# Performance work log

Hardware: AMD Instinct MI355X
Metric: run time of the kernel (lower is better)

## Reference

```python
import jax, jax.numpy as jnp
from jax import lax
import numpy as np

B, CIN, HC, K, REC = 64, 64, 64, 3, 5
MG = 240 // REC  # 48
EPS = 1e-8


def conv2d(x, w, b, pad):
    y = lax.conv_general_dilated(x, w, (1, 1), [(pad, pad), (pad, pad)],
                                 dimension_numbers=('NCHW', 'OIHW', 'NCHW'))
    return y + b[None, :, None, None]


def conv_transpose2d(x, w, b, stride, pad):
    # PyTorch ConvTranspose2d: w is (Cin, Cout, kH, kW)
    k = w.shape[2]
    w_t = jnp.transpose(w[:, :, ::-1, ::-1], (1, 0, 2, 3))  # -> OIHW, flipped
    y = lax.conv_general_dilated(x, w_t, (1, 1),
                                 [(k - 1 - pad, k - 1 - pad)] * 2,
                                 lhs_dilation=(stride, stride),
                                 dimension_numbers=('NCHW', 'OIHW', 'NCHW'))
    return y + b[None, :, None, None]


def leaky(x):
    return jnp.where(x >= 0, x, 0.2 * x)


def setup_inputs() -> dict:
    key = jax.random.key(0)
    ks = jax.random.split(key, 12)
    s = 0.05
    return {
        'x': jax.random.normal(ks[0], (B, CIN, 64, 64), jnp.float32),
        'h': jax.random.normal(ks[1], (B, HC, 64, 64), jnp.float32),
        'c': jax.random.normal(ks[2], (B, HC, 64, 64), jnp.float32),
        'recalled_memory_feature': jax.random.normal(ks[3], (B, REC, MG, 32, 32), jnp.float32),
        'conv_w': jax.random.normal(ks[4], (5 * HC, CIN + HC, K, K), jnp.float32) * s,
        'conv_b': jax.random.normal(ks[5], (5 * HC,), jnp.float32) * s,
        'convc_w': jax.random.normal(ks[6], (MG, HC, 1, 1), jnp.float32) * s,
        'convc_b': jax.random.normal(ks[7], (MG,), jnp.float32) * s,
        'convssm_w': jax.random.normal(ks[8], (MG, MG, 4, 4), jnp.float32) * s,
        'convssm_b': jax.random.normal(ks[9], (MG,), jnp.float32) * s,
        'convfuse_w': jax.random.normal(ks[10], (HC, MG + HC, 1, 1), jnp.float32) * s,
        'convfuse_b': jax.random.normal(ks[11], (HC,), jnp.float32) * s,
    }


def reference(x, h, c, recalled_memory_feature, conv_w, conv_b, convc_w, convc_b,
              convssm_w, convssm_b, convfuse_w, convfuse_b):
    rm = recalled_memory_feature.reshape(B, REC, MG, 32, 32)
    rm_avg = rm.mean(axis=(3, 4))                      # (B, REC, MG)
    q = leaky(conv2d(c, convc_w, convc_b, 0))          # (B, MG, 64, 64)
    q_avg = q.mean(axis=(2, 3))                        # (B, MG)
    # cosine similarity along channel dim, vectorized over (B, REC)
    qn = jnp.maximum(jnp.linalg.norm(q_avg, axis=1, keepdims=True), EPS)   # (B,1)
    mn = jnp.maximum(jnp.linalg.norm(rm_avg, axis=2), EPS)                  # (B,REC)
    cos = jnp.einsum('bm,brm->br', q_avg, rm_avg) / (qn * mn)               # (B,REC)
    attn = jax.nn.softmax(cos, axis=1)                                      # (B,REC)
    mt = jnp.einsum('br,brmhw->bmhw', attn, rm)        # (B, MG, 32, 32)
    mt = leaky(conv_transpose2d(mt, convssm_w, convssm_b, 2, 1))  # (B, MG, 64, 64)

    gates = conv2d(jnp.concatenate((x, h), axis=1), conv_w, conv_b, K // 2)
    i, f, g, o, lam = jnp.split(gates, 5, axis=1)
    i = jax.nn.sigmoid(i)
    f = jax.nn.sigmoid(f)
    o = jax.nn.sigmoid(o)
    g = jnp.tanh(g)
    lam = jax.nn.sigmoid(lam)
    c_new = f * c + i * g
    h_new = o * jnp.tanh(conv2d(jnp.concatenate((c_new, mt), axis=1), convfuse_w, convfuse_b, 0))
    h_out = lam * h_new + (1.0 - lam) * h
    return (h_out, c_new)
```

## Files before the change

### kernel.cpp

```cpp
#include <hip/hip_runtime.h>
#include <hip/hip_bf16.h>
#include <cstdint>

#define HW 4096
#define MGc 48
#define RECc 5

typedef __attribute__((ext_vector_type(8))) short bf16x8;
typedef __attribute__((ext_vector_type(4))) float f32x4;

__device__ __forceinline__ float sigf(float x) { return 1.f / (1.f + expf(-x)); }
__device__ __forceinline__ float leakyf(float x) { return x >= 0.f ? x : 0.2f * x; }
__device__ __forceinline__ unsigned short f2bfu(float f) {
  __hip_bfloat16 b = __float2bfloat16(f);
  return *reinterpret_cast<unsigned short*>(&b);
}
__device__ __forceinline__ float bfu2f(unsigned short u) {
  unsigned v = ((unsigned)u) << 16;
  return __uint_as_float(v);
}
__device__ __forceinline__ void gload_lds16(const void* g, void* l) {
  __builtin_amdgcn_global_load_lds(
      (const __attribute__((address_space(1))) unsigned int*)g,
      (__attribute__((address_space(3))) unsigned int*)l, 16, 0, 0);
}

__global__ __launch_bounds__(256) void k_rm_sum(const float* __restrict__ rm,
                                                float* __restrict__ rm_sum) {
  int row = blockIdx.x;
  const float4* p = reinterpret_cast<const float4*>(rm + (size_t)row * 1024);
  float4 v = p[threadIdx.x];
  float s = v.x + v.y + v.z + v.w;
  #pragma unroll
  for (int off = 32; off; off >>= 1) s += __shfl_down(s, off);
  __shared__ float sred[4];
  if ((threadIdx.x & 63) == 0) sred[threadIdx.x >> 6] = s;
  __syncthreads();
  if (threadIdx.x == 0) rm_sum[row] = sred[0] + sred[1] + sred[2] + sred[3];
}

__global__ __launch_bounds__(256) void k_q_part(const float* __restrict__ c,
    const float* __restrict__ ccw, const float* __restrict__ ccb,
    float* __restrict__ q_part) {
  __shared__ float wl[MGc * 64];
  __shared__ float bl[MGc];
  __shared__ float red[4][MGc];
  int b = blockIdx.y, seg = blockIdx.x;
  for (int i = threadIdx.x; i < MGc * 64; i += 256) wl[i] = ccw[i];
  if (threadIdx.x < MGc) bl[threadIdx.x] = ccb[threadIdx.x];
  __syncthreads();
  int px = seg * 256 + threadIdx.x;
  float acc[MGc];
  #pragma unroll
  for (int m = 0; m < MGc; m++) acc[m] = 0.f;
  const float* cp = c + (size_t)b * 64 * HW + px;
  for (int ci = 0; ci < 64; ci++) {
    float v = cp[(size_t)ci * HW];
    #pragma unroll
    for (int m = 0; m < MGc; m++) acc[m] += wl[m * 64 + ci] * v;
  }
  int lane = threadIdx.x & 63, wv = threadIdx.x >> 6;
  #pragma unroll
  for (int m = 0; m < MGc; m++) {
    float t = leakyf(acc[m] + bl[m]);
    #pragma unroll
    for (int off = 32; off; off >>= 1) t += __shfl_down(t, off);
    if (lane == 0) red[wv][m] = t;
  }
  __syncthreads();
  if (threadIdx.x < MGc) {
    float t = red[0][threadIdx.x] + red[1][threadIdx.x] + red[2][threadIdx.x] + red[3][threadIdx.x];
    q_part[((size_t)b * 16 + seg) * MGc + threadIdx.x] = t;
  }
}

__global__ __launch_bounds__(256) void k_mt_pre(const float* __restrict__ rm,
    const float* __restrict__ rm_sum, const float* __restrict__ q_part,
    float* __restrict__ mt_pre) {
  __shared__ float sat[RECc];
  int idx = blockIdx.x * 256 + threadIdx.x;
  int b = idx / (MGc * 1024);
  if (threadIdx.x < 64) {
    int lane = threadIdx.x;
    float q = 0.f;
    if (lane < MGc) {
      float s = 0.f;
      for (int sg = 0; sg < 16; sg++) s += q_part[((size_t)b * 16 + sg) * MGc + lane];
      q = s * (1.f / 4096.f);
    }
    float qs = q * q;
    #pragma unroll
    for (int off = 32; off; off >>= 1) qs += __shfl_xor(qs, off);
    float qn = fmaxf(sqrtf(qs), 1e-8f);
    float cosv[RECc];
    #pragma unroll
    for (int r = 0; r < RECc; r++) {
      float m = 0.f;
      if (lane < MGc) m = rm_sum[((size_t)b * RECc + r) * MGc + lane] * (1.f / 1024.f);
      float d = q * m, ms = m * m;
      #pragma unroll
      for (int off = 32; off; off >>= 1) { d += __shfl_xor(d, off); ms += __shfl_xor(ms, off); }
      float mn = fmaxf(sqrtf(ms), 1e-8f);
      cosv[r] = d / (qn * mn);
    }
    float mx = cosv[0];
    #pragma unroll
    for (int r = 1; r < RECc; r++) mx = fmaxf(mx, cosv[r]);
    float ssum = 0.f;
    #pragma unroll
    for (int r = 0; r < RECc; r++) { cosv[r] = expf(cosv[r] - mx); ssum += cosv[r]; }
    float inv = 1.f / ssum;
    #pragma unroll
    for (int r = 0; r < RECc; r++)
      if (lane == r) sat[r] = cosv[r] * inv;
  }
  __syncthreads();
  int rem = idx - b * (MGc * 1024);
  const float* base = rm + (size_t)b * RECc * MGc * 1024 + rem;
  float v = sat[0] * base[0] + sat[1] * base[MGc * 1024] + sat[2] * base[2 * MGc * 1024]
          + sat[3] * base[3 * MGc * 1024] + sat[4] * base[4 * MGc * 1024];
  mt_pre[idx] = v;
}

__global__ __launch_bounds__(512) void k_ssm(const float* __restrict__ mt_pre,
    const float* __restrict__ w, const float* __restrict__ bias,
    __hip_bfloat16* __restrict__ mt) {
  __shared__ float in_t[12][10][20];
  __shared__ float w_t[12][48][16];
  int b = blockIdx.y;
  int tile = blockIdx.x;
  int y0 = (tile >> 1) * 16, x0 = (tile & 1) * 32;
  int wv = threadIdx.x >> 6, lane = threadIdx.x & 63;
  int co0 = wv * 6;
  int oyl = lane >> 2, xseg = lane & 3;
  int oy = y0 + oyl;
  int iy0 = (y0 >> 1) - 1, ix0 = (x0 >> 1) - 1;
  int kyA = (oy + 1) & 1;
  int iyA = (oy + 1 - kyA) >> 1;
  int rA = iyA - iy0, rB = rA - 1;
  float acc[6][8] = {};
  for (int ch = 0; ch < 4; ch++) {
    int ci0 = ch * 12;
    __syncthreads();
    for (int i = threadIdx.x; i < 12 * 10 * 18; i += 512) {
      int ci = i / 180, rr = (i % 180) / 18, cc2 = i % 18;
      int giy = iy0 + rr, gix = ix0 + cc2;
      float v = 0.f;
      if ((unsigned)giy < 32u && (unsigned)gix < 32u)
        v = mt_pre[(((size_t)b * MGc + ci0 + ci) * 32 + giy) * 32 + gix];
      in_t[ci][rr][cc2] = v;
    }
    for (int i = threadIdx.x; i < 12 * 48 * 16; i += 512)
      (&w_t[0][0][0])[i] = w[ci0 * 768 + i];
    __syncthreads();
    #pragma unroll 1
    for (int ci = 0; ci < 12; ci++) {
      float4 a0 = *reinterpret_cast<const float4*>(&in_t[ci][rA][xseg * 4]);
      float4 a1 = *reinterpret_cast<const float4*>(&in_t[ci][rA][xseg * 4 + 4]);
      float4 b0 = *reinterpret_cast<const float4*>(&in_t[ci][rB][xseg * 4]);
      float4 b1 = *reinterpret_cast<const float4*>(&in_t[ci][rB][xseg * 4 + 4]);
      float vA[6] = {a0.x, a0.y, a0.z, a0.w, a1.x, a1.y};
      float vB[6] = {b0.x, b0.y, b0.z, b0.w, b1.x, b1.y};
      #pragma unroll
      for (int co = 0; co < 6; co++) {
        const float* wp = &w_t[ci][co0 + co][0];
        float4 wA = *reinterpret_cast<const float4*>(wp + kyA * 4);
        float4 wB = *reinterpret_cast<const float4*>(wp + (kyA + 2) * 4);
        #pragma unroll
        for (int j = 0; j < 8; j++) {
          if ((j & 1) == 0) {
            int hi = (j >> 1) + 1, lo = j >> 1;
            acc[co][j] += vA[hi] * wA.y + vA[lo] * wA.w + vB[hi] * wB.y + vB[lo] * wB.w;
          } else {
            int hi = ((j + 1) >> 1) + 1, lo = (j + 1) >> 1;
            acc[co][j] += vA[hi] * wA.x + vA[lo] * wA.z + vB[hi] * wB.x + vB[lo] * wB.z;
          }
        }
      }
    }
  }
  int oxb = x0 + xseg * 8;
  #pragma unroll
  for (int co = 0; co < 6; co++) {
    float bb = bias[co0 + co];
    size_t obase = (((size_t)b * MGc + co0 + co) * 64 + oy) * 64 + oxb;
    #pragma unroll
    for (int j = 0; j < 8; j++)
      mt[obase + j] = __float2bfloat16(leakyf(acc[co][j] + bb));
  }
}

__global__ __launch_bounds__(256) void k_ppack(const float* __restrict__ xin,
    const float* __restrict__ hin, __hip_bfloat16* __restrict__ P) {
  __shared__ float t[64][65];
  int b = blockIdx.z, y = blockIdx.y, half = blockIdx.x;
  const float* src = (half ? hin : xin) + (size_t)b * 64 * HW + y * 64;
  #pragma unroll
  for (int it = 0; it < 4; it++) {
    int li = it * 256 + threadIdx.x;
    int ci = li >> 4, x4 = (li & 15) * 4;
    float4 v = *reinterpret_cast<const float4*>(src + (size_t)ci * HW + x4);
    t[x4][ci] = v.x; t[x4 + 1][ci] = v.y; t[x4 + 2][ci] = v.z; t[x4 + 3][ci] = v.w;
  }
  __syncthreads();
  int x = threadIdx.x >> 2, c16 = (threadIdx.x & 3) * 16;
  unsigned short* dst = reinterpret_cast<unsigned short*>(P) +
      (((size_t)b * 4096 + (size_t)y * 64 + x) * 128 + half * 64 + c16);
  bf16x8 o0, o1;
  #pragma unroll
  for (int j = 0; j < 8; j++) {
    o0[j] = (short)f2bfu(t[x][c16 + j]);
    o1[j] = (short)f2bfu(t[x][c16 + 8 + j]);
  }
  *reinterpret_cast<bf16x8*>(dst) = o0;
  *reinterpret_cast<bf16x8*>(dst + 8) = o1;
}

__global__ __launch_bounds__(256) void k_wpack(const float* __restrict__ cw,
                                               __hip_bfloat16* __restrict__ Wp) {
  int idx = blockIdx.x * 256 + threadIdx.x;
  if (idx >= 9 * 320 * 128) return;
  int t = idx / (320 * 128);
  int rem = idx % (320 * 128);
  int ocp = rem / 128, ci = rem % 128;
  int nt = ocp / 80, r2 = ocp % 80, gate = r2 / 16, ml = r2 % 16;
  int oc = gate * 64 + nt * 16 + ml;
  float v = cw[((size_t)oc * 128 + ci) * 9 + t];
  Wp[idx] = __float2bfloat16(v);
}

__global__ __launch_bounds__(512) void k_gates_mfma(
    const __hip_bfloat16* __restrict__ P, const __hip_bfloat16* __restrict__ Wp,
    const float* __restrict__ c, const float* __restrict__ cb,
    float* __restrict__ c_new, __hip_bfloat16* __restrict__ o_g,
    __hip_bfloat16* __restrict__ lam_g) {
  __shared__ bf16x8 s_in[18 * 4 * 66];
  __shared__ bf16x8 s_w[9 * 4 * 80];
  int orig = blockIdx.y * gridDim.x + blockIdx.x;
  int t_id = (orig & 7) * 128 + (orig >> 3);
  int b = t_id >> 4;
  int ytile = (t_id >> 2) & 3, nt = t_id & 3;
  int y0 = ytile * 16;
  int tid = threadIdx.x;
  int wv = tid >> 6, lane = tid & 63;
  int wr = wv >> 2, xw = wv & 3;
  int lane15 = lane & 15, lq = lane >> 4;

  f32x4 acc[8][5];
  #pragma unroll
  for (int i = 0; i < 8; i++)
    #pragma unroll
    for (int j = 0; j < 5; j++) acc[i][j] = (f32x4)0.f;

  const char* Pb = (const char*)P;
  const char* Wb = (const char*)Wp;

  for (int cc = 0; cc < 4; cc++) {
    __syncthreads();
    #pragma unroll 1
    for (int u = wv; u < 72; u += 8) {
      int L = u >> 2, g = u & 3;
      int y = y0 - 1 + L;
      bf16x8* dst = &s_in[u * 66];
      if ((unsigned)y < 64u) {
        const char* gp = Pb + ((((size_t)b * 4096 + (size_t)y * 64 + lane) * 128) + cc * 32 + g * 8) * 2;
        gload_lds16(gp, (void*)(dst + 1));
        if (lane < 2) dst[lane * 65] = (bf16x8)0;
      } else {
        dst[lane] = (bf16x8)0;
        if (lane < 2) dst[64 + lane] = (bf16x8)0;
      }
    }
    #pragma unroll 1
    for (int u = wv; u < 45; u += 8) {
      int e = u * 64 + lane;
      int t = e / 320, rem = e % 320;
      int g = rem / 80, ol = rem % 80;
      const char* gp = Wb + (((size_t)t * 320 + nt * 80 + ol) * 128 + cc * 32 + g * 8) * 2;
      gload_lds16(gp, (void*)&s_w[e]);
    }
    __syncthreads();

    #pragma unroll
    for (int dx = 0; dx < 3; dx++) {
      bf16x8 af[10];
      #pragma unroll
      for (int ri = 0; ri < 10; ri++) {
        int L = wr * 8 + ri;
        af[ri] = s_in[(L * 4 + lq) * 66 + (xw * 16 + lane15 + dx)];
      }
      #pragma unroll
      for (int ky = 0; ky < 3; ky++) {
        int t = ky * 3 + dx;
        bf16x8 bw[5];
        #pragma unroll
        for (int gg = 0; gg < 5; gg++)
          bw[gg] = s_w[(t * 4 + lq) * 80 + gg * 16 + lane15];
        #pragma unroll
        for (int rr = 0; rr < 8; rr++) {
          #pragma unroll
          for (int gg = 0; gg < 5; gg++)
            acc[rr][gg] = __builtin_amdgcn_mfma_f32_16x16x32_bf16(
                af[rr + ky], bw[gg], acc[rr][gg], 0, 0, 0);
        }
      }
    }
  }

  int m_hid = nt * 16 + lane15;
  float bi = cb[m_hid], bff = cb[64 + m_hid], bgg = cb[128 + m_hid],
        bo = cb[192 + m_hid], bl = cb[256 + m_hid];
  int xb = xw * 16 + lq * 4;
  size_t chofs = ((size_t)b * 64 + m_hid) * HW;
  #pragma unroll
  for (int rr = 0; rr < 8; rr++) {
    int y = y0 + wr * 8 + rr;
    size_t pofs = chofs + (size_t)y * 64 + xb;
    f32x4 cold = *reinterpret_cast<const f32x4*>(c + pofs);
    f32x4 cn;
    unsigned short ov[4], lv[4];
    #pragma unroll
    for (int e = 0; e < 4; e++) {
      float i_ = sigf(acc[rr][0][e] + bi);
      float f_ = sigf(acc[rr][1][e] + bff);
      float g_ = tanhf(acc[rr][2][e] + bgg);
      float o_ = sigf(acc[rr][3][e] + bo);
      float l_ = sigf(acc[rr][4][e] + bl);
      cn[e] = f_ * cold[e] + i_ * g_;
      ov[e] = f2bfu(o_);
      lv[e] = f2bfu(l_);
    }
    *reinterpret_cast<f32x4*>(c_new + pofs) = cn;
    ushort4 ovv = {ov[0], ov[1], ov[2], ov[3]};
    ushort4 lvv = {lv[0], lv[1], lv[2], lv[3]};
    *reinterpret_cast<ushort4*>(reinterpret_cast<unsigned short*>(o_g) + pofs) = ovv;
    *reinterpret_cast<ushort4*>(reinterpret_cast<unsigned short*>(lam_g) + pofs) = lvv;
  }
}

__global__ __launch_bounds__(256) void k_fuse(const float* __restrict__ c_new,
    const __hip_bfloat16* __restrict__ mt, const __hip_bfloat16* __restrict__ o_g,
    const __hip_bfloat16* __restrict__ lam_g, const float* __restrict__ h,
    const float* __restrict__ fw, const float* __restrict__ fb,
    float* __restrict__ h_out) {
  __shared__ float wl[112][64];
  int b = blockIdx.y, seg = blockIdx.x;
  for (int i = threadIdx.x; i < 112 * 64; i += 256) {
    int ci = i >> 6, co = i & 63;
    wl[ci][co] = fw[co * 112 + ci];
  }
  __syncthreads();
  int px = seg * 512 + threadIdx.x * 2;
  size_t bofs = (size_t)b * 64 * HW;
  float2 acc[64];
  #pragma unroll
  for (int co = 0; co < 64; co++) { float bv = fb[co]; acc[co].x = bv; acc[co].y = bv; }
  #pragma unroll 1
  for (int ci = 0; ci < 64; ci++) {
    float2 v = *reinterpret_cast<const float2*>(c_new + bofs + (size_t)ci * HW + px);
    #pragma unroll
    for (int c4 = 0; c4 < 16; c4++) {
      float4 w = *reinterpret_cast<const float4*>(&wl[ci][c4 * 4]);
      acc[c4 * 4 + 0].x += w.x * v.x; acc[c4 * 4 + 0].y += w.x * v.y;
      acc[c4 * 4 + 1].x += w.y * v.x; acc[c4 * 4 + 1].y += w.y * v.y;
      acc[c4 * 4 + 2].x += w.z * v.x; acc[c4 * 4 + 2].y += w.z * v.y;
      acc[c4 * 4 + 3].x += w.w * v.x; acc[c4 * 4 + 3].y += w.w * v.y;
    }
  }
  const unsigned short* mtu = reinterpret_cast<const unsigned short*>(mt);
  size_t mtofs = (size_t)b * MGc * HW + px;
  #pragma unroll 1
  for (int ci = 0; ci < 48; ci++) {
    unsigned u = *reinterpret_cast<const unsigned*>(mtu + mtofs + (size_t)ci * HW);
    float vx = bfu2f((unsigned short)(u & 0xffff));
    float vy = bfu2f((unsigned short)(u >> 16));
    #pragma unroll
    for (int c4 = 0; c4 < 16; c4++) {
      float4 w = *reinterpret_cast<const float4*>(&wl[64 + ci][c4 * 4]);
      acc[c4 * 4 + 0].x += w.x * vx; acc[c4 * 4 + 0].y += w.x * vy;
      acc[c4 * 4 + 1].x += w.y * vx; acc[c4 * 4 + 1].y += w.y * vy;
      acc[c4 * 4 + 2].x += w.z * vx; acc[c4 * 4 + 2].y += w.z * vy;
      acc[c4 * 4 + 3].x += w.w * vx; acc[c4 * 4 + 3].y += w.w * vy;
    }
  }
  const unsigned short* ou = reinterpret_cast<const unsigned short*>(o_g);
  const unsigned short* lu = reinterpret_cast<const unsigned short*>(lam_g);
  #pragma unroll
  for (int co = 0; co < 64; co++) {
    size_t ofs = bofs + (size_t)co * HW + px;
    unsigned uo = *reinterpret_cast<const unsigned*>(ou + ofs);
    unsigned ul = *reinterpret_cast<const unsigned*>(lu + ofs);
    float2 hv = *reinterpret_cast<const float2*>(h + ofs);
    float hnx = tanhf(acc[co].x), hny = tanhf(acc[co].y);
    float ox = bfu2f((unsigned short)(uo & 0xffff)), oy = bfu2f((unsigned short)(uo >> 16));
    float lx = bfu2f((unsigned short)(ul & 0xffff)), ly = bfu2f((unsigned short)(ul >> 16));
    float2 r;
    r.x = lx * (ox * hnx) + (1.f - lx) * hv.x;
    r.y = ly * (oy * hny) + (1.f - ly) * hv.y;
    *reinterpret_cast<float2*>(h_out + ofs) = r;
  }
}

extern "C" void kernel_launch(void* const* d_in, const int* in_sizes, int n_in,
                              void* d_out, int out_size, void* d_ws, size_t ws_size,
                              hipStream_t stream) {
  const float* x   = (const float*)d_in[0];
  const float* h   = (const float*)d_in[1];
  const float* c   = (const float*)d_in[2];
  const float* rm  = (const float*)d_in[3];
  const float* cw  = (const float*)d_in[4];
  const float* cb  = (const float*)d_in[5];
  const float* ccw = (const float*)d_in[6];
  const float* ccb = (const float*)d_in[7];
  const float* sw  = (const float*)d_in[8];
  const float* sb  = (const float*)d_in[9];
  const float* fw  = (const float*)d_in[10];
  const float* fb  = (const float*)d_in[11];

  float* h_out = (float*)d_out;
  float* c_new = h_out + (size_t)16777216;

  char* ws = (char*)d_ws;
  float* rm_sum = (float*)(ws + 0);
  float* q_part = (float*)(ws + 65536);
  float* mt_pre = (float*)(ws + 327680);
  __hip_bfloat16* mt    = (__hip_bfloat16*)(ws + 12910592);
  __hip_bfloat16* o_g   = (__hip_bfloat16*)(ws + 38076416);
  __hip_bfloat16* lam_g = (__hip_bfloat16*)(ws + 71630848);
  __hip_bfloat16* P     = (__hip_bfloat16*)(ws + 105185280);
  __hip_bfloat16* Wp    = (__hip_bfloat16*)(ws + 172294144);

  k_wpack<<<1440, 256, 0, stream>>>(cw, Wp);
  k_ppack<<<dim3(2, 64, 64), 256, 0, stream>>>(x, h, P);
  k_rm_sum<<<15360, 256, 0, stream>>>(rm, rm_sum);
  k_q_part<<<dim3(16, 64), 256, 0, stream>>>(c, ccw, ccb, q_part);
  k_mt_pre<<<12288, 256, 0, stream>>>(rm, rm_sum, q_part, mt_pre);
  k_ssm<<<dim3(8, 64), 512, 0, stream>>>(mt_pre, sw, sb, mt);
  k_gates_mfma<<<dim3(16, 64), 512, 0, stream>>>(P, Wp, c, cb, c_new, o_g, lam_g);
  k_fuse<<<dim3(8, 64), 256, 0, stream>>>(c_new, mt, o_g, lam_g, h, fw, fb, h_out);
}
```

Baseline: 691.7 us.

## Double-buffer gates conv LDS staging with repacked tap-channel K dimension

Splits the channel reduction into eight 16-channel chunks staged into two LDS buffers, so the next chunk's global-to-LDS loads overlap MFMA compute on the current one. The K dimension of each MFMA is repacked to combine (tap, 8-channel group) pairs, with the final slot partially zeroed. MFMA bursts are wrapped in raised wave priority. This adds redundant zero MFMAs and more LDS fragment reads in exchange for hiding load latency.

```diff
diff --git a/kernel.cpp b/kernel.cpp
--- a/kernel.cpp
+++ b/kernel.cpp
@@ -234,8 +234,8 @@
     const float* __restrict__ c, const float* __restrict__ cb,
     float* __restrict__ c_new, __hip_bfloat16* __restrict__ o_g,
     __hip_bfloat16* __restrict__ lam_g) {
-  __shared__ bf16x8 s_in[18 * 4 * 66];
-  __shared__ bf16x8 s_w[9 * 4 * 80];
+  __shared__ bf16x8 s_in[2][36 * 66];
+  __shared__ bf16x8 s_w[2][18 * 80];
   int orig = blockIdx.y * gridDim.x + blockIdx.x;
   int t_id = (orig & 7) * 128 + (orig >> 3);
   int b = t_id >> 4;
@@ -245,6 +245,19 @@
   int wv = tid >> 6, lane = tid & 63;
   int wr = wv >> 2, xw = wv & 3;
   int lane15 = lane & 15, lq = lane >> 4;
+  int rowu = wr * 8;
+
+  int afq[5], bwq[5];
+  #pragma unroll
+  for (int q = 0; q < 5; q++) {
+    int j = q * 4 + lq;
+    int jj = (j < 18) ? j : (j - 2);
+    int t = jj >> 1, g = jj & 1;
+    int ky = t / 3, dx = t % 3;
+    afq[q] = ky * 132 + g * 66 + xw * 16 + lane15 + dx;
+    bwq[q] = (t * 2 + g) * 80 + lane15;
+  }
+  bool a4ok = (lq < 2);
 
   f32x4 acc[8][5];
   #pragma unroll
@@ -255,57 +268,72 @@
   const char* Pb = (const char*)P;
   const char* Wb = (const char*)Wp;
 
-  for (int cc = 0; cc < 4; cc++) {
+#define STAGE_K(BUF, CC) do {                                                         \
+    _Pragma("unroll 1")                                                               \
+    for (int u = wv; u < 36; u += 8) {                                                \
+      int L = u >> 1, g = u & 1;                                                      \
+      int y = y0 - 1 + L;                                                             \
+      bf16x8* dst = &s_in[BUF][u * 66];                                               \
+      if ((unsigned)y < 64u) {                                                        \
+        const char* gp = Pb + ((((size_t)b * 4096 + (size_t)y * 64 + lane) * 128)     \
+                               + (CC) * 16 + g * 8) * 2;                              \
+        gload_lds16(gp, (void*)(dst + 1));                                            \
+        if (lane < 2) dst[lane * 65] = (bf16x8)0;                                     \
+      } else {                                                                        \
+        dst[lane] = (bf16x8)0;                                                        \
+        if (lane < 2) dst[64 + lane] = (bf16x8)0;                                     \
+      }                                                                               \
+    }                                                                                 \
+    _Pragma("unroll 1")                                                               \
+    for (int u = wv; u < 23; u += 8) {                                                \
+      int e = u * 64 + lane;                                                          \
+      if (e < 1440) {                                                                 \
+        int unit = e / 80, ol = e % 80;                                               \
+        int t = unit >> 1, g = unit & 1;                                              \
+        const char* gp = Wb + (((size_t)t * 320 + nt * 80 + ol) * 128                 \
+                               + (CC) * 16 + g * 8) * 2;                              \
+        gload_lds16(gp, (void*)&s_w[BUF][e]);                                         \
+      }                                                                               \
+    }                                                                                 \
+  } while (0)
+
+#define COMPUTE_K(BUF) do {                                                           \
+    _Pragma("unroll")                                                                 \
+    for (int q = 0; q < 5; q++) {                                                     \
+      bf16x8 af[8];                                                                   \
+      _Pragma("unroll")                                                               \
+      for (int rr = 0; rr < 8; rr++) {                                                \
+        bf16x8 v = s_in[BUF][(rowu + rr) * 132 + afq[q]];                             \
+        af[rr] = (q < 4 || a4ok) ? v : (bf16x8)0;                                     \
+      }                                                                               \
+      bf16x8 bw[5];                                                                   \
+      _Pragma("unroll")                                                               \
+      for (int gg = 0; gg < 5; gg++) bw[gg] = s_w[BUF][bwq[q] + gg * 16];             \
+      __builtin_amdgcn_s_setprio(1);                                                  \
+      _Pragma("unroll")                                                               \
+      for (int rr = 0; rr < 8; rr++)                                                  \
+        _Pragma("unroll")                                                             \
+        for (int gg = 0; gg < 5; gg++)                                                \
+          acc[rr][gg] = __builtin_amdgcn_mfma_f32_16x16x32_bf16(                      \
+              af[rr], bw[gg], acc[rr][gg], 0, 0, 0);                                  \
+      __builtin_amdgcn_s_setprio(0);                                                  \
+    }                                                                                 \
+  } while (0)
+
+  STAGE_K(0, 0);
+  __syncthreads();
+  #pragma unroll 1
+  for (int cp = 0; cp < 4; cp++) {
+    int cc = cp * 2;
+    STAGE_K(1, cc + 1);
+    COMPUTE_K(0);
     __syncthreads();
-    #pragma unroll 1
-    for (int u = wv; u < 72; u += 8) {
-      int L = u >> 2, g = u & 3;
-      int y = y0 - 1 + L;
-      bf16x8* dst = &s_in[u * 66];
-      if ((unsigned)y < 64u) {
-        const char* gp = Pb + ((((size_t)b * 4096 + (size_t)y * 64 + lane) * 128) + cc * 32 + g * 8) * 2;
-        gload_lds16(gp, (void*)(dst + 1));
-        if (lane < 2) dst[lane * 65] = (bf16x8)0;
-      } else {
-        dst[lane] = (bf16x8)0;
-        if (lane < 2) dst[64 + lane] = (bf16x8)0;
-      }
-    }
-    #pragma unroll 1
-    for (int u = wv; u < 45; u += 8) {
-      int e = u * 64 + lane;
-      int t = e / 320, rem = e % 320;
-      int g = rem / 80, ol = rem % 80;
-      const char* gp = Wb + (((size_t)t * 320 + nt * 80 + ol) * 128 + cc * 32 + g * 8) * 2;
-      gload_lds16(gp, (void*)&s_w[e]);
-    }
+    if (cp < 3) STAGE_K(0, cc + 2);
+    COMPUTE_K(1);
     __syncthreads();
-
-    #pragma unroll
-    for (int dx = 0; dx < 3; dx++) {
-      bf16x8 af[10];
-      #pragma unroll
-      for (int ri = 0; ri < 10; ri++) {
-        int L = wr * 8 + ri;
-        af[ri] = s_in[(L * 4 + lq) * 66 + (xw * 16 + lane15 + dx)];
-      }
-      #pragma unroll
-      for (int ky = 0; ky < 3; ky++) {
-        int t = ky * 3 + dx;
-        bf16x8 bw[5];
-        #pragma unroll
-        for (int gg = 0; gg < 5; gg++)
-          bw[gg] = s_w[(t * 4 + lq) * 80 + gg * 16 + lane15];
-        #pragma unroll
-        for (int rr = 0; rr < 8; rr++) {
-          #pragma unroll
-          for (int gg = 0; gg < 5; gg++)
-            acc[rr][gg] = __builtin_amdgcn_mfma_f32_16x16x32_bf16(
-                af[rr + ky], bw[gg], acc[rr][gg], 0, 0, 0);
-        }
-      }
-    }
-  }
+  }
+#undef STAGE_K
+#undef COMPUTE_K
 
   int m_hid = nt * 16 + lane15;
   float bi = cb[m_hid], bff = cb[64 + m_hid], bgg = cb[128 + m_hid],
```

After: 785.9 us. +13.6%, slower.

## Load gate-conv input fragments directly from padded global layout, skip LDS staging

Applied to the files above, without the earlier changes.

The packed x/h input is rewritten into a zero-padded 66x66 spatial layout. A new prep kernel packs the weights and zeroes the padding borders, so the gates MFMA kernel no longer needs bounds checks or an LDS input tile. That kernel now reads A fragments straight from global memory into registers, with a two-buffer prefetch across the three dx shifts, and raises wave priority around the MFMA bursts. The aim is to cut LDS traffic and barrier-bound staging, at the cost of repeated global/L2 reads of overlapping fragments and a larger padded buffer; workspace buffers are also re-laid out to reuse regions that are no longer live.

```diff
diff --git a/kernel.cpp b/kernel.cpp
--- a/kernel.cpp
+++ b/kernel.cpp
@@ -23,6 +23,35 @@
   __builtin_amdgcn_global_load_lds(
       (const __attribute__((address_space(1))) unsigned int*)g,
       (__attribute__((address_space(3))) unsigned int*)l, 16, 0, 0);
+}
+
+__global__ __launch_bounds__(256) void k_prep(const float* __restrict__ cw,
+    __hip_bfloat16* __restrict__ Wp, __hip_bfloat16* __restrict__ Pp) {
+  if (blockIdx.x < 1440) {
+    int idx = blockIdx.x * 256 + threadIdx.x;
+    int t = idx / (320 * 128);
+    int rem = idx % (320 * 128);
+    int ocp = rem / 128, ci = rem % 128;
+    int nt = ocp / 80, r2 = ocp % 80, gate = r2 / 16, ml = r2 % 16;
+    int oc = gate * 64 + nt * 16 + ml;
+    Wp[idx] = __float2bfloat16(cw[((size_t)oc * 128 + ci) * 9 + t]);
+  } else {
+    int idx = (blockIdx.x - 1440) * 256 + threadIdx.x;
+    int b = idx / 4160, i = idx % 4160;
+    bf16x8* base = reinterpret_cast<bf16x8*>(Pp);
+    size_t u;
+    if (i < 2112) {
+      int r = (i < 1056) ? 0 : 65;
+      int j = (i < 1056) ? i : i - 1056;
+      u = ((size_t)b * 66 + r) * 1056 + j;
+    } else {
+      int i2 = i - 2112;
+      int row = 1 + (i2 >> 5), k = i2 & 31;
+      int px = (k < 16) ? 0 : 65, ci8 = k & 15;
+      u = (((size_t)b * 66 + row) * 66 + px) * 16 + ci8;
+    }
+    base[u] = (bf16x8)0;
+  }
 }
 
 __global__ __launch_bounds__(256) void k_rm_sum(const float* __restrict__ rm,
@@ -191,7 +220,7 @@
 }
 
 __global__ __launch_bounds__(256) void k_ppack(const float* __restrict__ xin,
-    const float* __restrict__ hin, __hip_bfloat16* __restrict__ P) {
+    const float* __restrict__ hin, __hip_bfloat16* __restrict__ Pp) {
   __shared__ float t[64][65];
   int b = blockIdx.z, y = blockIdx.y, half = blockIdx.x;
   const float* src = (half ? hin : xin) + (size_t)b * 64 * HW + y * 64;
@@ -204,8 +233,8 @@
   }
   __syncthreads();
   int x = threadIdx.x >> 2, c16 = (threadIdx.x & 3) * 16;
-  unsigned short* dst = reinterpret_cast<unsigned short*>(P) +
-      (((size_t)b * 4096 + (size_t)y * 64 + x) * 128 + half * 64 + c16);
+  unsigned short* dst = reinterpret_cast<unsigned short*>(Pp) +
+      ((((size_t)b * 66 + y + 1) * 66 + x + 1) * 128 + half * 64 + c16);
   bf16x8 o0, o1;
   #pragma unroll
   for (int j = 0; j < 8; j++) {
@@ -216,25 +245,11 @@
   *reinterpret_cast<bf16x8*>(dst + 8) = o1;
 }
 
-__global__ __launch_bounds__(256) void k_wpack(const float* __restrict__ cw,
-                                               __hip_bfloat16* __restrict__ Wp) {
-  int idx = blockIdx.x * 256 + threadIdx.x;
-  if (idx >= 9 * 320 * 128) return;
-  int t = idx / (320 * 128);
-  int rem = idx % (320 * 128);
-  int ocp = rem / 128, ci = rem % 128;
-  int nt = ocp / 80, r2 = ocp % 80, gate = r2 / 16, ml = r2 % 16;
-  int oc = gate * 64 + nt * 16 + ml;
-  float v = cw[((size_t)oc * 128 + ci) * 9 + t];
-  Wp[idx] = __float2bfloat16(v);
-}
-
 __global__ __launch_bounds__(512) void k_gates_mfma(
-    const __hip_bfloat16* __restrict__ P, const __hip_bfloat16* __restrict__ Wp,
+    const __hip_bfloat16* __restrict__ Pp, const __hip_bfloat16* __restrict__ Wp,
     const float* __restrict__ c, const float* __restrict__ cb,
     float* __restrict__ c_new, __hip_bfloat16* __restrict__ o_g,
     __hip_bfloat16* __restrict__ lam_g) {
-  __shared__ bf16x8 s_in[18 * 4 * 66];
   __shared__ bf16x8 s_w[9 * 4 * 80];
   int orig = blockIdx.y * gridDim.x + blockIdx.x;
   int t_id = (orig & 7) * 128 + (orig >> 3);
@@ -246,31 +261,38 @@
   int wr = wv >> 2, xw = wv & 3;
   int lane15 = lane & 15, lq = lane >> 4;
 
+  const char* Ab = (const char*)Pp +
+      ((((size_t)b * 66 + (y0 + wr * 8)) * 66 + (xw * 16 + lane15)) * 256) + lq * 16;
+
   f32x4 acc[8][5];
   #pragma unroll
   for (int i = 0; i < 8; i++)
     #pragma unroll
     for (int j = 0; j < 5; j++) acc[i][j] = (f32x4)0.f;
 
-  const char* Pb = (const char*)P;
   const char* Wb = (const char*)Wp;
 
+#define COMP(AF, DX) do {                                                             \
+    _Pragma("unroll")                                                                 \
+    for (int ky = 0; ky < 3; ky++) {                                                  \
+      int t = ky * 3 + (DX);                                                          \
+      bf16x8 bw[5];                                                                   \
+      _Pragma("unroll")                                                               \
+      for (int gg = 0; gg < 5; gg++) bw[gg] = s_w[(t * 4 + lq) * 80 + gg * 16 + lane15]; \
+      __builtin_amdgcn_s_setprio(1);                                                  \
+      _Pragma("unroll")                                                               \
+      for (int rr = 0; rr < 8; rr++)                                                  \
+        _Pragma("unroll")                                                             \
+        for (int gg = 0; gg < 5; gg++)                                                \
+          acc[rr][gg] = __builtin_amdgcn_mfma_f32_16x16x32_bf16(                      \
+              AF[rr + ky], bw[gg], acc[rr][gg], 0, 0, 0);                             \
+      __builtin_amdgcn_s_setprio(0);                                                  \
+    }                                                                                 \
+  } while (0)
+
+  #pragma unroll 1
   for (int cc = 0; cc < 4; cc++) {
     __syncthreads();
-    #pragma unroll 1
-    for (int u = wv; u < 72; u += 8) {
-      int L = u >> 2, g = u & 3;
-      int y = y0 - 1 + L;
-      bf16x8* dst = &s_in[u * 66];
-      if ((unsigned)y < 64u) {
-        const char* gp = Pb + ((((size_t)b * 4096 + (size_t)y * 64 + lane) * 128) + cc * 32 + g * 8) * 2;
-        gload_lds16(gp, (void*)(dst + 1));
-        if (lane < 2) dst[lane * 65] = (bf16x8)0;
-      } else {
-        dst[lane] = (bf16x8)0;
-        if (lane < 2) dst[64 + lane] = (bf16x8)0;
-      }
-    }
     #pragma unroll 1
     for (int u = wv; u < 45; u += 8) {
       int e = u * 64 + lane;
@@ -279,33 +301,23 @@
       const char* gp = Wb + (((size_t)t * 320 + nt * 80 + ol) * 128 + cc * 32 + g * 8) * 2;
       gload_lds16(gp, (void*)&s_w[e]);
     }
+    const char* Ac = Ab + cc * 64;
+    bf16x8 afA[10], afB[10];
+    #pragma unroll
+    for (int ri = 0; ri < 10; ri++)
+      afA[ri] = *reinterpret_cast<const bf16x8*>(Ac + ri * 16896);
     __syncthreads();
-
-    #pragma unroll
-    for (int dx = 0; dx < 3; dx++) {
-      bf16x8 af[10];
-      #pragma unroll
-      for (int ri = 0; ri < 10; ri++) {
-        int L = wr * 8 + ri;
-        af[ri] = s_in[(L * 4 + lq) * 66 + (xw * 16 + lane15 + dx)];
-      }
-      #pragma unroll
-      for (int ky = 0; ky < 3; ky++) {
-        int t = ky * 3 + dx;
-        bf16x8 bw[5];
-        #pragma unroll
-        for (int gg = 0; gg < 5; gg++)
-          bw[gg] = s_w[(t * 4 + lq) * 80 + gg * 16 + lane15];
-        #pragma unroll
-        for (int rr = 0; rr < 8; rr++) {
-          #pragma unroll
-          for (int gg = 0; gg < 5; gg++)
-            acc[rr][gg] = __builtin_amdgcn_mfma_f32_16x16x32_bf16(
-                af[rr + ky], bw[gg], acc[rr][gg], 0, 0, 0);
-        }
-      }
-    }
-  }
+    #pragma unroll
+    for (int ri = 0; ri < 10; ri++)
+      afB[ri] = *reinterpret_cast<const bf16x8*>(Ac + ri * 16896 + 256);
+    COMP(afA, 0);
+    #pragma unroll
+    for (int ri = 0; ri < 10; ri++)
+      afA[ri] = *reinterpret_cast<const bf16x8*>(Ac + ri * 16896 + 512);
+    COMP(afB, 1);
+    COMP(afA, 2);
+  }
+#undef COMP
 
   int m_hid = nt * 16 + lane15;
   float bi = cb[m_hid], bff = cb[64 + m_hid], bgg = cb[128 + m_hid],
@@ -423,19 +435,19 @@
   char* ws = (char*)d_ws;
   float* rm_sum = (float*)(ws + 0);
   float* q_part = (float*)(ws + 65536);
-  float* mt_pre = (float*)(ws + 327680);
-  __hip_bfloat16* mt    = (__hip_bfloat16*)(ws + 12910592);
-  __hip_bfloat16* o_g   = (__hip_bfloat16*)(ws + 38076416);
-  __hip_bfloat16* lam_g = (__hip_bfloat16*)(ws + 71630848);
-  __hip_bfloat16* P     = (__hip_bfloat16*)(ws + 105185280);
-  __hip_bfloat16* Wp    = (__hip_bfloat16*)(ws + 172294144);
-
-  k_wpack<<<1440, 256, 0, stream>>>(cw, Wp);
-  k_ppack<<<dim3(2, 64, 64), 256, 0, stream>>>(x, h, P);
+  float* mt_pre = (float*)(ws + 262144);
+  __hip_bfloat16* o_g   = (__hip_bfloat16*)(ws + 0);
+  __hip_bfloat16* lam_g = (__hip_bfloat16*)(ws + 33554432);
+  __hip_bfloat16* mt    = (__hip_bfloat16*)(ws + 67108864);
+  __hip_bfloat16* Pp    = (__hip_bfloat16*)(ws + 92274688);
+  __hip_bfloat16* Wp    = (__hip_bfloat16*)(ws + 163643392);
+
+  k_prep<<<2480, 256, 0, stream>>>(cw, Wp, Pp);
+  k_ppack<<<dim3(2, 64, 64), 256, 0, stream>>>(x, h, Pp);
   k_rm_sum<<<15360, 256, 0, stream>>>(rm, rm_sum);
   k_q_part<<<dim3(16, 64), 256, 0, stream>>>(c, ccw, ccb, q_part);
   k_mt_pre<<<12288, 256, 0, stream>>>(rm, rm_sum, q_part, mt_pre);
   k_ssm<<<dim3(8, 64), 512, 0, stream>>>(mt_pre, sw, sb, mt);
-  k_gates_mfma<<<dim3(16, 64), 512, 0, stream>>>(P, Wp, c, cb, c_new, o_g, lam_g);
+  k_gates_mfma<<<dim3(16, 64), 512, 0, stream>>>(Pp, Wp, c, cb, c_new, o_g, lam_g);
   k_fuse<<<dim3(8, 64), 256, 0, stream>>>(c_new, mt, o_g, lam_g, h, fw, fb, h_out);
 }
```

New measurement: 783.7 us. 1.13x slower.
